# Kernel optimization log

Measured on AMD Instinct MI355X. Metric: run time of the kernel, lower is better.

The kernel has to match this reference:

```python
import jax, jax.numpy as jnp
import numpy as np

EPS = 1e-06

def rmsnorm(x, w):
    x32 = x.astype(jnp.float32)
    var = jnp.mean(x32 * x32, axis=-1, keepdims=True)
    return w * (x32 * jax.lax.rsqrt(var + EPS)).astype(x.dtype)

def setup_inputs() -> dict:
    B, T, C = 16, 256, 16
    token_dim, text_dim = 1024, 512
    key = jax.random.key(0)
    ks = jax.random.split(key, 8)
    token_embeds = jax.random.normal(ks[0], (B, T, token_dim), dtype=jnp.float32)
    char_embeds = jax.random.normal(ks[1], (B, T, C, text_dim), dtype=jnp.float32)
    filler_embed = jax.random.normal(ks[2], (text_dim,), dtype=jnp.float32)
    mask = jax.random.randint(ks[3], (B, T, C), 0, 2).astype(bool)
    mask = mask.at[0].set(True)  # force max valid count == T*C (static output shape)
    token_ids_mask = jnp.ones((B, T), dtype=bool)
    # xavier-uniform-ish weights
    def xav(k, fan_out, fan_in, gain=1.0):
        lim = gain * np.sqrt(6.0 / (fan_in + fan_out))
        return jax.random.uniform(k, (fan_out, fan_in), jnp.float32, -lim, lim)
    W_down = xav(ks[4], text_dim, token_dim)
    W_proj = xav(ks[5], 3, text_dim, gain=0.2)
    W_fusion = xav(ks[6], text_dim, text_dim)
    w_pre = jnp.ones((token_dim,), jnp.float32)
    w_tok = jnp.ones((text_dim,), jnp.float32)
    w_char = jnp.ones((text_dim,), jnp.float32)
    return {"token_embeds": token_embeds, "token_ids_mask": token_ids_mask,
            "char_embeds": char_embeds, "char_ids_mask": mask,
            "filler_embed": filler_embed, "w_pre": w_pre, "w_tok": w_tok,
            "w_char": w_char, "W_down": W_down, "W_proj": W_proj,
            "W_fusion": W_fusion, "max_valid_chars": T * C}

def reference(token_embeds, token_ids_mask, char_embeds, char_ids_mask,
              filler_embed, w_pre, w_tok, w_char, W_down, W_proj, W_fusion,
              max_valid_chars):
    B, T, C, d = char_embeds.shape
    MV = int(max_valid_chars)
    tok = rmsnorm(token_embeds, w_pre)                       # [B,T,token_dim]
    feats = rmsnorm(jnp.einsum('btk,dk->btd', tok, W_down), w_tok)  # [B,T,d]
    params = jnp.einsum('btd,pd->btp', jax.nn.silu(feats), W_proj)  # [B,T,3]
    scale = params[..., 0][:, :, None, None]                 # [B,T,1,1]
    shift = params[..., 1][:, :, None, None]
    gate = jax.nn.sigmoid(params[..., 2][:, :, None, None])
    cn = rmsnorm(char_embeds, w_char)                        # [B,T,C,d]
    fused = jnp.einsum('btcd,ed->btce', jax.nn.silu(cn * (1.0 + scale) + shift), W_fusion)
    fused = gate * fused + (1.0 - gate) * cn                 # [B,T,C,d]
    flat = fused.reshape(B, T * C, d)
    m = char_ids_mask.reshape(B, T * C).astype(jnp.int32)
    pos = jnp.cumsum(m, axis=1) - 1                          # dest within row
    offs = jnp.arange(B, dtype=jnp.int32)[:, None] * MV
    idx = jnp.where(m > 0, offs + pos, B * MV)               # invalid -> dump slot
    buf = jnp.broadcast_to(filler_embed, (B * MV + 1, d))
    buf = buf.at[idx.reshape(-1)].set(flat.reshape(-1, d))
    return buf[: B * MV].reshape(B, MV, d)
```

## Files before the change

### kernel.cpp

```cpp
#include <hip/hip_runtime.h>
#include <cstdint>
#include <cstddef>

#define EPS 1e-6f

typedef short bf16x8 __attribute__((ext_vector_type(8)));
typedef float f32x4  __attribute__((ext_vector_type(4)));

__device__ __forceinline__ short f2bf(float x) {
    uint32_t u = __builtin_bit_cast(uint32_t, x);
    return (short)((u + 0x7FFFu + ((u >> 16) & 1u)) >> 16);
}

__global__ __launch_bounds__(256) void k_front(
    const void* __restrict__ maskp, int* __restrict__ v_list, int* __restrict__ counts,
    const float* __restrict__ Wf, short* __restrict__ Wfbf,
    const float* __restrict__ Wd, short* __restrict__ Wdbf,
    const float* __restrict__ tokens, const float* __restrict__ w_pre,
    short* __restrict__ tokbf) {
    const int blk = blockIdx.x, tid = threadIdx.x;
    if (blk < 16) {
        __shared__ int wtot[4], woff[4];
        __shared__ int mode_s;
        const int b = blk, lane = tid & 63, wave = tid >> 6;
        if (tid == 0) mode_s = 0;
        __syncthreads();
        {
            int bad = 0;
#pragma unroll
            for (int q = 0; q < 4; ++q)
                bad |= (((const uint32_t*)maskp)[q * 256 + tid] > 1u) ? 1 : 0;
            if (bad) mode_s = 1;
        }
        __syncthreads();
        int f[16];
        if (mode_s) {
            const uint4 v = ((const uint4*)maskp)[(b << 8) + tid];
            const uint32_t ws[4] = {v.x, v.y, v.z, v.w};
#pragma unroll
            for (int q = 0; q < 4; ++q) {
                f[q * 4 + 0] = (ws[q] & 0x000000ffu) != 0;
                f[q * 4 + 1] = (ws[q] & 0x0000ff00u) != 0;
                f[q * 4 + 2] = (ws[q] & 0x00ff0000u) != 0;
                f[q * 4 + 3] = (ws[q] & 0xff000000u) != 0;
            }
        } else {
            const uint4* mp = (const uint4*)maskp + ((size_t)b << 10) + tid * 4;
#pragma unroll
            for (int q = 0; q < 4; ++q) {
                const uint4 v = mp[q];
                f[q * 4 + 0] = v.x != 0; f[q * 4 + 1] = v.y != 0;
                f[q * 4 + 2] = v.z != 0; f[q * 4 + 3] = v.w != 0;
            }
        }
        int c = 0;
#pragma unroll
        for (int q = 0; q < 16; ++q) c += f[q];
        int incl = c;
#pragma unroll
        for (int off = 1; off < 64; off <<= 1) {
            const int n = __shfl_up(incl, off);
            if (lane >= off) incl += n;
        }
        if (lane == 63) wtot[wave] = incl;
        __syncthreads();
        if (tid == 0) {
            int run = 0;
#pragma unroll
            for (int wv = 0; wv < 4; ++wv) { woff[wv] = run; run += wtot[wv]; }
            counts[b] = run;
        }
        __syncthreads();
        int base = woff[wave] + incl - c;
        int* vl = v_list + (b << 12);
        const int i0 = tid * 16;
#pragma unroll
        for (int q = 0; q < 16; ++q)
            if (f[q]) vl[base++] = i0 + q;
    } else if (blk < 784) {
        const int gid = (blk - 16) * 256 + tid;
        const float* s; short* d; int i;
        if (gid < 65536) { s = Wf; d = Wfbf; i = gid; }
        else             { s = Wd; d = Wdbf; i = gid - 65536; }
        const float4 v = ((const float4*)s)[i];
        short4 o;
        o.x = f2bf(v.x); o.y = f2bf(v.y); o.z = f2bf(v.z); o.w = f2bf(v.w);
        ((short4*)d)[i] = o;
    } else {
        const int lane = tid & 63, wave = tid >> 6;
        const int row = (blk - 784) * 4 + wave;
        const float* xp = tokens + (size_t)row * 1024 + lane * 16;
        float4 x[4];
#pragma unroll
        for (int q = 0; q < 4; ++q) x[q] = *(const float4*)&xp[q * 4];
        float ss = 0.f;
#pragma unroll
        for (int q = 0; q < 4; ++q)
            ss += x[q].x * x[q].x + x[q].y * x[q].y + x[q].z * x[q].z + x[q].w * x[q].w;
#pragma unroll
        for (int off = 32; off > 0; off >>= 1) ss += __shfl_down(ss, off);
        ss = __shfl(ss, 0);
        const float r = rsqrtf(ss * (1.0f / 1024.0f) + EPS);
        const float* wp = w_pre + lane * 16;
        short* op = tokbf + (size_t)row * 1024 + lane * 16;
#pragma unroll
        for (int h = 0; h < 2; ++h) {
            bf16x8 o;
#pragma unroll
            for (int q = 0; q < 2; ++q) {
                const float4 wv = *(const float4*)&wp[h * 8 + q * 4];
                const float4 xv = x[h * 2 + q];
                o[q * 4 + 0] = f2bf(xv.x * wv.x * r);
                o[q * 4 + 1] = f2bf(xv.y * wv.y * r);
                o[q * 4 + 2] = f2bf(xv.z * wv.z * r);
                o[q * 4 + 3] = f2bf(xv.w * wv.w * r);
            }
            *(bf16x8*)&op[h * 8] = o;
        }
    }
}

__global__ __launch_bounds__(256) void k_gemm_tok(const short* __restrict__ tokbf,
                                                  const short* __restrict__ Wdbf,
                                                  float* __restrict__ feats) {
    __shared__ short As[2][128 * 32];
    __shared__ short Bs[2][128 * 32];
    const int tid = threadIdx.x, lane = tid & 63, w = tid >> 6;
    const int kt = blockIdx.x >> 7;
    const int mt = (blockIdx.x >> 2) & 31, nt = blockIdx.x & 3;
    const int wm = w >> 1, wn = w & 1;
    const int kbase = kt * 512;
    const short* hA = tokbf + (size_t)mt * 128 * 1024;
    const short* wB = Wdbf + (size_t)nt * 128 * 1024;

    f32x4 acc[4][4];
#pragma unroll
    for (int mi = 0; mi < 4; ++mi)
#pragma unroll
        for (int ni = 0; ni < 4; ++ni) acc[mi][ni] = (f32x4)0.f;

    const int rA = lane & 15, ch = lane >> 4;

    auto STAGE = [&](int bufi, int kk) {
#pragma unroll
        for (int q = 0; q < 2; ++q) {
            const int cid = (w * 2 + q) * 64 + lane;
            const int r = cid >> 2, kc = cid & 3;
            const int kcs = kc ^ ((r >> 1) & 3);
            const size_t go = (size_t)r * 1024 + kk + kcs * 8;
            __builtin_amdgcn_global_load_lds(
                (const __attribute__((address_space(1))) uint32_t*)(hA + go),
                (__attribute__((address_space(3))) uint32_t*)&As[bufi][(w * 2 + q) * 512], 16, 0, 0);
            __builtin_amdgcn_global_load_lds(
                (const __attribute__((address_space(1))) uint32_t*)(wB + go),
                (__attribute__((address_space(3))) uint32_t*)&Bs[bufi][(w * 2 + q) * 512], 16, 0, 0);
        }
    };
    auto COMPUTE = [&](int bufi) {
        bf16x8 af[4], bfr[4];
#pragma unroll
        for (int mi = 0; mi < 4; ++mi) {
            const int row = wm * 64 + mi * 16 + rA;
            af[mi] = *(const bf16x8*)&As[bufi][row * 32 + ((ch ^ ((row >> 1) & 3)) << 3)];
        }
#pragma unroll
        for (int ni = 0; ni < 4; ++ni) {
            const int row = wn * 64 + ni * 16 + rA;
            bfr[ni] = *(const bf16x8*)&Bs[bufi][row * 32 + ((ch ^ ((row >> 1) & 3)) << 3)];
        }
#pragma unroll
        for (int mi = 0; mi < 4; ++mi)
#pragma unroll
            for (int ni = 0; ni < 4; ++ni)
                acc[mi][ni] = __builtin_amdgcn_mfma_f32_16x16x32_bf16(af[mi], bfr[ni], acc[mi][ni], 0, 0, 0);
    };

    STAGE(0, kbase);
    __syncthreads();
    for (int kk = 0; kk < 512; kk += 64) {
        STAGE(1, kbase + kk + 32);
        COMPUTE(0);
        __syncthreads();
        if (kk + 64 < 512) STAGE(0, kbase + kk + 64);
        COMPUTE(1);
        __syncthreads();
    }

    float* fo = feats + (size_t)kt * 4096 * 512;
    const int rowb = mt * 128 + wm * 64 + (lane >> 4) * 4;
    const int colb = nt * 128 + wn * 64 + (lane & 15);
#pragma unroll
    for (int mi = 0; mi < 4; ++mi)
#pragma unroll
        for (int ni = 0; ni < 4; ++ni)
#pragma unroll
            for (int rg = 0; rg < 4; ++rg)
                fo[(size_t)(rowb + mi * 16 + rg) * 512 + colb + ni * 16] = acc[mi][ni][rg];
}

__global__ __launch_bounds__(64) void k_params(
    const float* __restrict__ feats_pre, const float* __restrict__ w_tok,
    const float* __restrict__ W_proj, float* __restrict__ params) {
    const int tk = blockIdx.x;
    const int lane = threadIdx.x;
    const int d0 = lane * 8;
    const float* fp0 = feats_pre + (size_t)tk * 512 + d0;
    const float* fp1 = fp0 + (size_t)4096 * 512;
    const float4 a0 = *(const float4*)&fp0[0];
    const float4 a1 = *(const float4*)&fp0[4];
    const float4 b0 = *(const float4*)&fp1[0];
    const float4 b1 = *(const float4*)&fp1[4];
    const float4 f0 = make_float4(a0.x + b0.x, a0.y + b0.y, a0.z + b0.z, a0.w + b0.w);
    const float4 f1 = make_float4(a1.x + b1.x, a1.y + b1.y, a1.z + b1.z, a1.w + b1.w);
    float ss = f0.x * f0.x + f0.y * f0.y + f0.z * f0.z + f0.w * f0.w
             + f1.x * f1.x + f1.y * f1.y + f1.z * f1.z + f1.w * f1.w;
#pragma unroll
    for (int off = 32; off > 0; off >>= 1) ss += __shfl_down(ss, off);
    ss = __shfl(ss, 0);
    const float rms = rsqrtf(ss * (1.0f / 512.0f) + EPS);

    const float4 wt0 = *(const float4*)&w_tok[d0];
    const float4 wt1 = *(const float4*)&w_tok[d0 + 4];
    float fv[8] = {f0.x, f0.y, f0.z, f0.w, f1.x, f1.y, f1.z, f1.w};
    float wv[8] = {wt0.x, wt0.y, wt0.z, wt0.w, wt1.x, wt1.y, wt1.z, wt1.w};
    float s[8];
#pragma unroll
    for (int j = 0; j < 8; ++j) {
        const float v = fv[j] * wv[j] * rms;
        s[j] = v / (1.0f + expf(-v));
    }
    float p[3];
#pragma unroll
    for (int q = 0; q < 3; ++q) {
        const float* Wp = W_proj + (size_t)q * 512 + d0;
        const float4 a = *(const float4*)&Wp[0];
        const float4 c = *(const float4*)&Wp[4];
        p[q] = s[0] * a.x + s[1] * a.y + s[2] * a.z + s[3] * a.w
             + s[4] * c.x + s[5] * c.y + s[6] * c.z + s[7] * c.w;
#pragma unroll
        for (int off = 32; off > 0; off >>= 1) p[q] += __shfl_down(p[q], off);
    }
    if (lane == 0) {
        float* po = params + (size_t)tk * 4;
        po[0] = 1.0f + p[0];
        po[1] = p[1];
        po[2] = 1.0f / (1.0f + expf(-p[2]));
        po[3] = 0.f;
    }
}

__global__ __launch_bounds__(256) void k_prep(
    const float* __restrict__ chars, const float* __restrict__ w_char,
    const float* __restrict__ params, const int* __restrict__ v_list,
    const int* __restrict__ counts, short* __restrict__ hb,
    float* __restrict__ rms_l, float* __restrict__ g_l) {
    const int tid = threadIdx.x, lane = tid & 63, wave = tid >> 6;
    const int b = blockIdx.x >> 10;
    const int j = (blockIdx.x & 1023) * 4 + wave;
    const int cnt = counts[b];
    const int cpad = (cnt + 127) & ~127;
    if (j >= cpad) return;
    short* hrow = hb + ((size_t)(b << 12) + j) * 512 + lane * 8;
    if (j >= cnt) {
        *(bf16x8*)hrow = (bf16x8)0;
        return;
    }
    const int i = v_list[(b << 12) + j];
    const float* xp = chars + ((size_t)(b << 12) + i) * 512 + lane * 8;
    const float4 x0 = *(const float4*)&xp[0];
    const float4 x1 = *(const float4*)&xp[4];
    float ss = x0.x * x0.x + x0.y * x0.y + x0.z * x0.z + x0.w * x0.w
             + x1.x * x1.x + x1.y * x1.y + x1.z * x1.z + x1.w * x1.w;
#pragma unroll
    for (int off = 32; off > 0; off >>= 1) ss += __shfl_down(ss, off);
    ss = __shfl(ss, 0);
    const float rms = rsqrtf(ss * (1.0f / 512.0f) + EPS);
    const float* pp = params + (size_t)((b << 8) + (i >> 4)) * 4;
    const float s1 = pp[0], sh = pp[1], g = pp[2];
    const float4 w0 = *(const float4*)&w_char[lane * 8];
    const float4 w1 = *(const float4*)&w_char[lane * 8 + 4];
    float xv[8] = {x0.x, x0.y, x0.z, x0.w, x1.x, x1.y, x1.z, x1.w};
    float wv[8] = {w0.x, w0.y, w0.z, w0.w, w1.x, w1.y, w1.z, w1.w};
    bf16x8 o;
#pragma unroll
    for (int q = 0; q < 8; ++q) {
        const float cn = wv[q] * xv[q] * rms;
        const float a = cn * s1 + sh;
        o[q] = f2bf(a / (1.0f + expf(-a)));
    }
    *(bf16x8*)hrow = o;
    if (lane == 0) {
        rms_l[(b << 12) + j] = rms;
        g_l[(b << 12) + j] = g;
    }
}

__global__ __launch_bounds__(256) void k_gemm_fus(
    const short* __restrict__ hb, const short* __restrict__ Wbf,
    const float* __restrict__ chars, const float* __restrict__ w_char,
    const float* __restrict__ rms_l, const float* __restrict__ g_l,
    const int* __restrict__ v_list, const int* __restrict__ counts,
    const float* __restrict__ filler, float* __restrict__ out) {
    const int wg = (blockIdx.x & 7) * 256 + (blockIdx.x >> 3);
    const int b = wg >> 7;
    const int mt = (wg >> 2) & 31;
    const int nt = wg & 3;
    const int tid = threadIdx.x, lane = tid & 63, w = tid >> 6;
    const int cnt = counts[b];
    const int row0 = mt * 128;
    if (row0 >= cnt) {
        const int colb0 = nt * 128;
        const float4 f = *(const float4*)(filler + colb0 + (tid & 31) * 4);
        float* o0 = out + ((size_t)(b << 12) + row0) * 512 + colb0 + (tid & 31) * 4;
        for (int r = tid >> 5; r < 128; r += 8)
            *(float4*)&o0[(size_t)r * 512] = f;
        return;
    }

    __shared__ short As[2][128 * 32];
    __shared__ short Bs[2][128 * 32];
    __shared__ float g_s[128], rms_s[128];
    __shared__ int idx_s[128];
    const int wm = w >> 1, wn = w & 1;

    if (tid < 128) {
        const int j = row0 + tid;
        const bool valid = j < cnt;
        idx_s[tid] = valid ? v_list[(b << 12) + j] : 0;
        g_s[tid]   = valid ? g_l[(b << 12) + j] : 0.f;
        rms_s[tid] = valid ? rms_l[(b << 12) + j] : 0.f;
    }

    const short* hA = hb + ((size_t)(b << 12) + row0) * 512;
    const short* wB = Wbf + (size_t)nt * 128 * 512;

    f32x4 acc[4][4];
#pragma unroll
    for (int mi = 0; mi < 4; ++mi)
#pragma unroll
        for (int ni = 0; ni < 4; ++ni) acc[mi][ni] = (f32x4)0.f;

    const int rA = lane & 15, ch = lane >> 4;

    auto STAGE = [&](int bufi, int kk) {
#pragma unroll
        for (int q = 0; q < 2; ++q) {
            const int cid = (w * 2 + q) * 64 + lane;
            const int r = cid >> 2, kc = cid & 3;
            const int kcs = kc ^ ((r >> 1) & 3);
            const size_t go = (size_t)r * 512 + kk + kcs * 8;
            __builtin_amdgcn_global_load_lds(
                (const __attribute__((address_space(1))) uint32_t*)(hA + go),
                (__attribute__((address_space(3))) uint32_t*)&As[bufi][(w * 2 + q) * 512], 16, 0, 0);
            __builtin_amdgcn_global_load_lds(
                (const __attribute__((address_space(1))) uint32_t*)(wB + go),
                (__attribute__((address_space(3))) uint32_t*)&Bs[bufi][(w * 2 + q) * 512], 16, 0, 0);
        }
    };
    auto COMPUTE = [&](int bufi) {
        bf16x8 af[4], bfr[4];
#pragma unroll
        for (int mi = 0; mi < 4; ++mi) {
            const int row = wm * 64 + mi * 16 + rA;
            af[mi] = *(const bf16x8*)&As[bufi][row * 32 + ((ch ^ ((row >> 1) & 3)) << 3)];
        }
#pragma unroll
        for (int ni = 0; ni < 4; ++ni) {
            const int row = wn * 64 + ni * 16 + rA;
            bfr[ni] = *(const bf16x8*)&Bs[bufi][row * 32 + ((ch ^ ((row >> 1) & 3)) << 3)];
        }
#pragma unroll
        for (int mi = 0; mi < 4; ++mi)
#pragma unroll
            for (int ni = 0; ni < 4; ++ni)
                acc[mi][ni] = __builtin_amdgcn_mfma_f32_16x16x32_bf16(af[mi], bfr[ni], acc[mi][ni], 0, 0, 0);
    };

    STAGE(0, 0);
    __syncthreads();
    for (int kk = 0; kk < 512; kk += 64) {
        STAGE(1, kk + 32);
        COMPUTE(0);
        __syncthreads();
        if (kk + 64 < 512) STAGE(0, kk + 64);
        COMPUTE(1);
        __syncthreads();
    }

    const int colb = nt * 128 + wn * 64 + (lane & 15);
    float wcv[4];
#pragma unroll
    for (int ni = 0; ni < 4; ++ni) wcv[ni] = w_char[colb + ni * 16];
#pragma unroll
    for (int mi = 0; mi < 4; ++mi) {
#pragma unroll
        for (int rg = 0; rg < 4; ++rg) {
            const int jl = wm * 64 + mi * 16 + (lane >> 4) * 4 + rg;
            const int j = row0 + jl;
            const size_t orow = ((size_t)(b << 12) + j) * 512;
            if (j < cnt) {
                const float g = g_s[jl], rm = rms_s[jl];
                const size_t xrow = ((size_t)(b << 12) + idx_s[jl]) * 512;
#pragma unroll
                for (int ni = 0; ni < 4; ++ni) {
                    const int col = colb + ni * 16;
                    const float x = chars[xrow + col];
                    const float cn = wcv[ni] * x * rm;
                    out[orow + col] = g * acc[mi][ni][rg] + (1.0f - g) * cn;
                }
            } else {
#pragma unroll
                for (int ni = 0; ni < 4; ++ni) {
                    const int col = colb + ni * 16;
                    out[orow + col] = filler[col];
                }
            }
        }
    }
}

extern "C" void kernel_launch(void* const* d_in, const int* in_sizes, int n_in,
                              void* d_out, int out_size, void* d_ws, size_t ws_size,
                              hipStream_t stream) {
    const float* tokens = (const float*)d_in[0];
    const float* chars  = (const float*)d_in[2];
    const void*  cmask  = d_in[3];
    const float* filler = (const float*)d_in[4];
    const float* w_pre  = (const float*)d_in[5];
    const float* w_tok  = (const float*)d_in[6];
    const float* w_char = (const float*)d_in[7];
    const float* W_down = (const float*)d_in[8];
    const float* W_proj = (const float*)d_in[9];
    const float* W_fus  = (const float*)d_in[10];
    float* out = (float*)d_out;

    float* feats_pre = (float*)d_ws;
    float* params    = feats_pre + (size_t)2 * 4096 * 512;
    int*   counts    = (int*)(params + (size_t)4096 * 4);
    int*   v_list    = counts + 16;
    float* rms_l     = (float*)(v_list + 65536);
    float* g_l       = rms_l + 65536;
    short* Wbf       = (short*)(g_l + 65536);
    short* hb        = Wbf + (size_t)512 * 512;
    short* tokbf     = hb + (size_t)16 * 4096 * 512;
    short* Wdbf      = tokbf + (size_t)4096 * 1024;

    k_front<<<1808, 256, 0, stream>>>(cmask, v_list, counts, W_fus, Wbf,
                                      W_down, Wdbf, tokens, w_pre, tokbf);
    k_gemm_tok<<<256, 256, 0, stream>>>(tokbf, Wdbf, feats_pre);
    k_params<<<4096, 64, 0, stream>>>(feats_pre, w_tok, W_proj, params);
    k_prep<<<16384, 256, 0, stream>>>(chars, w_char, params, v_list, counts, hb, rms_l, g_l);
    k_gemm_fus<<<2048, 256, 0, stream>>>(hb, Wbf, chars, w_char, rms_l, g_l,
                                         v_list, counts, filler, out);
}
```

Measured before the change: 340.3 us.

## Deepen GEMM prefetch pipeline with vmcnt waits and pack k_params blocks

Both GEMM kernels now issue two K-stages up front and run a fully unrolled 16-step loop. Each step waits on vmcnt for only the older loads, so the next stage's global loads can overlap the current MFMA compute instead of sitting behind a full __syncthreads drain. In the fusion GEMM, the per-row index, gate and rms loads into shared memory move after the initial prefetches so they overlap with them. k_params packs four tokens per 256-thread block to cut the block count. The hand-written waitcnt values depend on the exact number of loads STAGE issues, which makes them fragile if the compiler reorders or splits those loads.

Measured after the change: 337.5 us. No clear change (-0.8%).

```diff
diff --git a/kernel.cpp b/kernel.cpp
--- a/kernel.cpp
+++ b/kernel.cpp
@@ -176,14 +176,19 @@
     };
 
     STAGE(0, kbase);
+    STAGE(1, kbase + 32);
     __syncthreads();
-    for (int kk = 0; kk < 512; kk += 64) {
-        STAGE(1, kbase + kk + 32);
-        COMPUTE(0);
-        __syncthreads();
-        if (kk + 64 < 512) STAGE(0, kbase + kk + 64);
-        COMPUTE(1);
-        __syncthreads();
+#pragma unroll
+    for (int t = 0; t < 16; ++t) {
+        if (t >= 2) {
+            if (t < 15) asm volatile("s_waitcnt vmcnt(4)" ::: "memory");
+            else        asm volatile("s_waitcnt vmcnt(0)" ::: "memory");
+            __builtin_amdgcn_sched_barrier(0);
+        }
+        __builtin_amdgcn_s_barrier();
+        COMPUTE(t & 1);
+        __builtin_amdgcn_s_barrier();
+        if (t < 14) STAGE(t & 1, kbase + (t + 2) * 32);
     }
 
     float* fo = feats + (size_t)kt * 4096 * 512;
@@ -198,11 +203,11 @@
                 fo[(size_t)(rowb + mi * 16 + rg) * 512 + colb + ni * 16] = acc[mi][ni][rg];
 }
 
-__global__ __launch_bounds__(64) void k_params(
+__global__ __launch_bounds__(256) void k_params(
     const float* __restrict__ feats_pre, const float* __restrict__ w_tok,
     const float* __restrict__ W_proj, float* __restrict__ params) {
-    const int tk = blockIdx.x;
-    const int lane = threadIdx.x;
+    const int tk = blockIdx.x * 4 + (threadIdx.x >> 6);
+    const int lane = threadIdx.x & 63;
     const int d0 = lane * 8;
     const float* fp0 = feats_pre + (size_t)tk * 512 + d0;
     const float* fp1 = fp0 + (size_t)4096 * 512;
@@ -323,14 +328,6 @@
     __shared__ int idx_s[128];
     const int wm = w >> 1, wn = w & 1;
 
-    if (tid < 128) {
-        const int j = row0 + tid;
-        const bool valid = j < cnt;
-        idx_s[tid] = valid ? v_list[(b << 12) + j] : 0;
-        g_s[tid]   = valid ? g_l[(b << 12) + j] : 0.f;
-        rms_s[tid] = valid ? rms_l[(b << 12) + j] : 0.f;
-    }
-
     const short* hA = hb + ((size_t)(b << 12) + row0) * 512;
     const short* wB = Wbf + (size_t)nt * 128 * 512;
 
@@ -377,14 +374,26 @@
     };
 
     STAGE(0, 0);
+    STAGE(1, 32);
+    if (tid < 128) {
+        const int j = row0 + tid;
+        const bool valid = j < cnt;
+        idx_s[tid] = valid ? v_list[(b << 12) + j] : 0;
+        g_s[tid]   = valid ? g_l[(b << 12) + j] : 0.f;
+        rms_s[tid] = valid ? rms_l[(b << 12) + j] : 0.f;
+    }
     __syncthreads();
-    for (int kk = 0; kk < 512; kk += 64) {
-        STAGE(1, kk + 32);
-        COMPUTE(0);
-        __syncthreads();
-        if (kk + 64 < 512) STAGE(0, kk + 64);
-        COMPUTE(1);
-        __syncthreads();
+#pragma unroll
+    for (int t = 0; t < 16; ++t) {
+        if (t >= 2) {
+            if (t < 15) asm volatile("s_waitcnt vmcnt(4)" ::: "memory");
+            else        asm volatile("s_waitcnt vmcnt(0)" ::: "memory");
+            __builtin_amdgcn_sched_barrier(0);
+        }
+        __builtin_amdgcn_s_barrier();
+        COMPUTE(t & 1);
+        __builtin_amdgcn_s_barrier();
+        if (t < 14) STAGE(t & 1, (t + 2) * 32);
     }
 
     const int colb = nt * 128 + wn * 64 + (lane & 15);
@@ -448,7 +457,7 @@
     k_front<<<1808, 256, 0, stream>>>(cmask, v_list, counts, W_fus, Wbf,
                                       W_down, Wdbf, tokens, w_pre, tokbf);
     k_gemm_tok<<<256, 256, 0, stream>>>(tokbf, Wdbf, feats_pre);
-    k_params<<<4096, 64, 0, stream>>>(feats_pre, w_tok, W_proj, params);
+    k_params<<<1024, 256, 0, stream>>>(feats_pre, w_tok, W_proj, params);
     k_prep<<<16384, 256, 0, stream>>>(chars, w_char, params, v_list, counts, hb, rms_l, g_l);
     k_gemm_fus<<<2048, 256, 0, stream>>>(hb, Wbf, chars, w_char, rms_l, g_l,
                                          v_list, counts, filler, out);
```
